# Optimization experiments

Measured on AMD Instinct MI355X. Metric: run time of the kernel, lower is better.

Reference implementation:

```python
import jax, jax.numpy as jnp
import numpy as np

# Module config (mirrors SWTLayer(__init__) with dimensions=[64,64,16], kmax=[3,3], wavelet='db1')
DIMS = (64, 64)      # spatial sizes along axes 1,2
LEVELS = (6, 6)      # pywt.dwt_max_level(64, dec_len=2) == 6 (Haar)
KMAX = (3, 3)
NLIFT = 16
BATCH = 32


def swt_haar(x, level, axis):
    """pywt.swt(x, 'db1', level, trim_approx=True, norm=True) along `axis` (periodic).
    norm=True Haar level-j step s=2^(j-1): cA[i]=(a[i]+a[i+s])/2, cD[i]=(a[i]-a[i+s])/2.
    Returns concat([cA_n, cD_n, ..., cD_1]) along axis (length (level+1)*M)."""
    a = x
    details = []
    for j in range(level):
        s = 2 ** j
        sh = jnp.roll(a, -s, axis)   # a[i + s] (periodic)
        details.append((a - sh) * 0.5)
        a = (a + sh) * 0.5
    return jnp.concatenate([a] + details[::-1], axis=axis)


def iswt_haar(xt, level, axis):
    """pywt.iswt inverse of swt_haar: averages the two phase reconstructions per level."""
    bands = jnp.split(xt, level + 1, axis=axis)  # [cA_n, cD_n, ..., cD_1]
    a = bands[0]
    for j in range(level, 0, -1):
        cD = bands[level - j + 1]
        s = 2 ** (j - 1)
        a = 0.5 * ((a + cD) + jnp.roll(a - cD, s, axis))
    return a


def setup_inputs() -> dict:
    key = jax.random.key(0)
    k1, k2, k3 = jax.random.split(key, 3)
    x = jax.random.normal(k1, (BATCH, DIMS[0], DIMS[1], NLIFT), dtype=jnp.float32)
    W = jax.random.uniform(
        k2,
        (NLIFT, NLIFT, DIMS[0] * (LEVELS[0] + 1), DIMS[1] * (LEVELS[1] + 1)),
        dtype=jnp.float32,
    )
    b = jax.random.normal(k3, (NLIFT, NLIFT), dtype=jnp.float32)
    return {"x": x, "weights": W, "bias": b}


def reference(x, weights, bias):
    # forward SWT along each spatial axis -> (B, 448, 448, C)
    xt = x
    for i, L in enumerate(LEVELS):
        xt = swt_haar(xt, L, axis=i + 1)
    # truncate: zero wavenumber bands [kmax*M, level*M) along each spatial axis
    for i, (M, L, K) in enumerate(zip(DIMS, LEVELS, KMAX)):
        idx = (slice(None),) * (i + 1) + (slice(K * M, L * M),)
        xt = xt.at[idx].set(0.0)
    # per-location channel mixing: 'abcd,debc->abce'
    xt = jnp.einsum('abcd,debc->abce', xt, weights)
    # inverse SWT back to (B, 64, 64, C)
    out = xt
    for i, L in enumerate(LEVELS):
        out = iswt_haar(out, L, axis=i + 1)
    # skip path: F.linear(x, bias) == x @ bias.T
    return out + x @ bias.T
```

## Files before the change

### kernel.cpp

```cpp
#include <hip/hip_runtime.h>
#include <cstddef>
#include <cstdint>


#define X1_IDX(a,u,j,d) ((((size_t)(a)*256 + (u))*64 + (j))*16 + (d))

__global__ __launch_bounds__(64) void k_swt1(const float* __restrict__ x,
                                             float* __restrict__ X1) {
  const int tid = threadIdx.x;
  const int d = tid & 15, jl = tid >> 4;
  const int a = blockIdx.x;
  const int j = blockIdx.y * 4 + jl;
  __shared__ float col[64 * 64];
  const float* xp = x + ((size_t)a * 4096 + j) * 16 + d;
  float S = 0.f;
  for (int i = 0; i < 64; ++i) {
    float v = xp[(size_t)i * 1024];
    col[i * 64 + tid] = v;
    S += v;
  }
  const float cA = S * 0.015625f;
  float w4 = 0.f, w4b = 0.f;
  for (int t = 0; t < 16; ++t)  w4  += col[t * 64 + tid];
  for (int t = 16; t < 32; ++t) w4b += col[t * 64 + tid];
  float w5 = w4 + w4b;
  float* X1p = X1 + X1_IDX(a, 0, j, d);
  for (int u = 0; u < 64; ++u) {
    const float c0 = col[u * 64 + tid];
    const float c16 = col[((u + 16) & 63) * 64 + tid];
    const float c32 = col[((u + 32) & 63) * 64 + tid];
    const float c1 = col[((u + 1) & 63) * 64 + tid];
    X1p[(size_t)(u) * 1024]        = cA;
    X1p[(size_t)(64 + u) * 1024]   = w5 * 0.03125f - cA;
    X1p[(size_t)(128 + u) * 1024]  = (w4 - w4b) * 0.03125f;
    X1p[(size_t)(192 + u) * 1024]  = (c0 - c1) * 0.5f;
    w4 += c16 - c0;
    w4b += c32 - c16;
    w5 += c32 - c0;
  }
}

#define APB 8
#define TS_STRIDE 4104
#define TS(a,v,d) ((a) * TS_STRIDE + (v) * 16 + (d))
#define WL_STRIDE 264

__global__ __launch_bounds__(256, 1) void k_fused(float* __restrict__ X1,
                                                  const float* __restrict__ W) {
  const int t = threadIdx.x;
  const int a0 = blockIdx.x * APB;
  const int u = blockIdx.y;
  const int ub = u >> 6;
  const int Brow = (ub == 3 ? 6 : ub) * 64 + (u & 63);
  __shared__ float Ts[APB * TS_STRIDE];
  __shared__ float Wl[16 * WL_STRIDE];

  if (t < 128) {
    const int a = t >> 4, d = t & 15;
    const float* xp = X1 + X1_IDX(a0 + a, u, 0, d);
    float raw[64];
    float S = 0.f, w4 = 0.f, w4b = 0.f;
#pragma unroll
    for (int j = 0; j < 64; ++j) {
      raw[j] = xp[j * 16];
      S += raw[j];
    }
#pragma unroll
    for (int j = 0; j < 16; ++j) w4 += raw[j];
#pragma unroll
    for (int j = 16; j < 32; ++j) w4b += raw[j];
    const float cA = S * 0.015625f;
    float w5 = w4 + w4b;
#pragma unroll
    for (int v = 0; v < 64; ++v) {
      Ts[TS(a, v, d)]       = cA;
      Ts[TS(a, 64 + v, d)]  = w5 * 0.03125f - cA;
      Ts[TS(a, 128 + v, d)] = (w4 - w4b) * 0.03125f;
      Ts[TS(a, 192 + v, d)] = (raw[v] - raw[(v + 1) & 63]) * 0.5f;
      const float c0 = raw[v], c16 = raw[(v + 16) & 63], c32 = raw[(v + 32) & 63];
      w4 += c16 - c0;
      w4b += c32 - c16;
      w5 += c32 - c0;
    }
  }
  __syncthreads();

  const int vl = t >> 4, e = t & 15;
  const float* wbase = W + (size_t)t * 200704 + (size_t)Brow * 448;
  for (int vg = 0; vg < 16; ++vg) {
    const int kb = vg >> 2;
    const int Ccol = (kb == 3 ? 6 : kb) * 64 + (vg & 3) * 16;
    __syncthreads();
    {
      const float* wp = wbase + Ccol;
#pragma unroll
      for (int i = 0; i < 16; i += 4) {
        float4 wv = *(const float4*)(wp + i);
        Wl[(i + 0) * WL_STRIDE + t] = wv.x;
        Wl[(i + 1) * WL_STRIDE + t] = wv.y;
        Wl[(i + 2) * WL_STRIDE + t] = wv.z;
        Wl[(i + 3) * WL_STRIDE + t] = wv.w;
      }
    }
    __syncthreads();
    const int v = vg * 16 + vl;
    float wreg[16];
#pragma unroll
    for (int d = 0; d < 16; ++d) wreg[d] = Wl[vl * WL_STRIDE + d * 16 + e];
#pragma unroll
    for (int a = 0; a < APB; ++a) {
      const float4 t0 = *(const float4*)&Ts[TS(a, v, 0)];
      const float4 t1 = *(const float4*)&Ts[TS(a, v, 4)];
      const float4 t2 = *(const float4*)&Ts[TS(a, v, 8)];
      const float4 t3 = *(const float4*)&Ts[TS(a, v, 12)];
      float acc = t0.x * wreg[0] + t0.y * wreg[1] + t0.z * wreg[2] + t0.w * wreg[3]
                + t1.x * wreg[4] + t1.y * wreg[5] + t1.z * wreg[6] + t1.w * wreg[7]
                + t2.x * wreg[8] + t2.y * wreg[9] + t2.z * wreg[10] + t2.w * wreg[11]
                + t3.x * wreg[12] + t3.y * wreg[13] + t3.z * wreg[14] + t3.w * wreg[15];
      Ts[TS(a, v, e)] = acc;
    }
  }
  __syncthreads();

  if (t < 128) {
    const int a = t >> 4, ee = t & 15;
    const float cA = Ts[TS(a, 0, ee)];
    float d6[64];
#pragma unroll
    for (int i = 0; i < 64; ++i) d6[i] = Ts[TS(a, 64 + i, ee)];
    float b6[64];
#pragma unroll
    for (int i = 0; i < 64; ++i) b6[i] = cA + 0.5f * (d6[i] - d6[(i - 32) & 63]);
    float d5[64];
#pragma unroll
    for (int i = 0; i < 64; ++i) d5[i] = Ts[TS(a, 128 + i, ee)];
    float a5[64];
#pragma unroll
    for (int i = 0; i < 64; ++i)
      a5[i] = 0.5f * (b6[i] + d5[i] + b6[(i - 16) & 63] - d5[(i - 16) & 63]);
    float b4[64];
#pragma unroll
    for (int i = 0; i < 64; ++i) b4[i] = 0.5f * (a5[i] + a5[(i - 8) & 63]);
    float a3[64];
#pragma unroll
    for (int i = 0; i < 64; ++i) a3[i] = 0.5f * (b4[i] + b4[(i - 4) & 63]);
    float b2[64];
#pragma unroll
    for (int i = 0; i < 64; ++i) b2[i] = 0.5f * (a3[i] + a3[(i - 2) & 63]);
    float d1[64];
#pragma unroll
    for (int i = 0; i < 64; ++i) d1[i] = Ts[TS(a, 192 + i, ee)];
    float* zp = X1 + X1_IDX(a0 + a, u, 0, ee);
#pragma unroll
    for (int j = 0; j < 64; ++j)
      zp[j * 16] = 0.5f * (b2[j] + d1[j] + b2[(j - 1) & 63] - d1[(j - 1) & 63]);
  }
}

__global__ __launch_bounds__(64) void k_iswt1(const float* __restrict__ Z1,
                                              const float* __restrict__ x,
                                              const float* __restrict__ bias,
                                              float* __restrict__ out) {
  const int tid = threadIdx.x, e = tid & 15, jl = tid >> 4;
  const int a = blockIdx.x, j = blockIdx.y * 4 + jl;
  __shared__ float A[64 * 64], Bv[64 * 64];
  __shared__ float bs[256];
  for (int i = tid; i < 256; i += 64) bs[i] = bias[i];
  __syncthreads();
  const float* Zp = Z1 + (size_t)a * 262144 + (size_t)j * 16 + e;
  for (int i = 0; i < 64; ++i) A[i * 64 + tid] = Zp[(size_t)i * 1024];
  for (int i = 0; i < 64; ++i) {
    float D = Zp[(size_t)(64 + i) * 1024];
    float D2 = Zp[(size_t)(64 + ((i - 32) & 63)) * 1024];
    Bv[i * 64 + tid] = 0.5f * (A[i * 64 + tid] + D + A[((i - 32) & 63) * 64 + tid] - D2);
  }
  for (int i = 0; i < 64; ++i) {
    float D = Zp[(size_t)(128 + i) * 1024];
    float D2 = Zp[(size_t)(128 + ((i - 16) & 63)) * 1024];
    A[i * 64 + tid] = 0.5f * (Bv[i * 64 + tid] + D + Bv[((i - 16) & 63) * 64 + tid] - D2);
  }
  for (int i = 0; i < 64; ++i)
    Bv[i * 64 + tid] = 0.5f * (A[i * 64 + tid] + A[((i - 8) & 63) * 64 + tid]);
  for (int i = 0; i < 64; ++i)
    A[i * 64 + tid] = 0.5f * (Bv[i * 64 + tid] + Bv[((i - 4) & 63) * 64 + tid]);
  for (int i = 0; i < 64; ++i)
    Bv[i * 64 + tid] = 0.5f * (A[i * 64 + tid] + A[((i - 2) & 63) * 64 + tid]);
  const float* xp = x + ((size_t)a * 4096 + j) * 16;
  float* op = out + ((size_t)a * 4096 + j) * 16 + e;
  for (int i = 0; i < 64; ++i) {
    float D = Zp[(size_t)(192 + i) * 1024];
    float D2 = Zp[(size_t)(192 + ((i - 1) & 63)) * 1024];
    float r = 0.5f * (Bv[i * 64 + tid] + D + Bv[((i - 1) & 63) * 64 + tid] - D2);
    float s = 0.f;
#pragma unroll
    for (int dd = 0; dd < 16; ++dd) s += xp[(size_t)i * 1024 + dd] * bs[e * 16 + dd];
    op[(size_t)i * 1024] = r + s;
  }
}

extern "C" void kernel_launch(void* const* d_in, const int* in_sizes, int n_in,
                              void* d_out, int out_size, void* d_ws, size_t ws_size,
                              hipStream_t stream) {
  const float* x = (const float*)d_in[0];
  const float* W = (const float*)d_in[1];
  const float* bias = (const float*)d_in[2];
  float* out = (float*)d_out;
  float* X1 = (float*)d_ws;

  k_swt1<<<dim3(32, 16), 64, 0, stream>>>(x, X1);
  k_fused<<<dim3(4, 256), 256, 0, stream>>>(X1, W);
  k_iswt1<<<dim3(32, 16), 64, 0, stream>>>(X1, x, bias, out);
}
```

Baseline: 401.7 us.

## Parallelize all three kernels across 256 threads and double-buffer weight loads

All three kernels are restructured. The SWT and ISWT kernels now split the 64-row transform across four thread groups of 256 threads, with partial sums shared through LDS. The fused kernel drops from 8 to 2 batch elements per block, uses a 4096-block grid with a remapped block index so blocks reuse W rows, and prefetches the next weight tile into registers while double-buffering it in LDS. The per-thread 64-register inverse transform is replaced by cooperative LDS passes, and the level 4-2 averaging collapses into an 8-tap sum. This targets low occupancy and idle threads, at the cost of more barriers and more redundant W loads per batch element.

```diff
diff --git a/kernel.cpp b/kernel.cpp
--- a/kernel.cpp
+++ b/kernel.cpp
@@ -5,196 +5,279 @@
 
 #define X1_IDX(a,u,j,d) ((((size_t)(a)*256 + (u))*64 + (j))*16 + (d))
 
-__global__ __launch_bounds__(64) void k_swt1(const float* __restrict__ x,
-                                             float* __restrict__ X1) {
-  const int tid = threadIdx.x;
-  const int d = tid & 15, jl = tid >> 4;
-  const int a = blockIdx.x;
-  const int j = blockIdx.y * 4 + jl;
+__global__ __launch_bounds__(256, 2) void k_swt1(const float* __restrict__ x,
+                                                 float* __restrict__ X1) {
   __shared__ float col[64 * 64];
-  const float* xp = x + ((size_t)a * 4096 + j) * 16 + d;
-  float S = 0.f;
-  for (int i = 0; i < 64; ++i) {
-    float v = xp[(size_t)i * 1024];
-    col[i * 64 + tid] = v;
-    S += v;
-  }
-  const float cA = S * 0.015625f;
-  float w4 = 0.f, w4b = 0.f;
-  for (int t = 0; t < 16; ++t)  w4  += col[t * 64 + tid];
-  for (int t = 16; t < 32; ++t) w4b += col[t * 64 + tid];
+  __shared__ float Ps[4][64];
+  const int t = threadIdx.x;
+  const int q = t >> 6, c = t & 63, jl = c >> 4, d = c & 15;
+  const int a = blockIdx.x, j = blockIdx.y * 4 + jl;
+  const float* xp = x + ((size_t)a * 4096 + j) * 16 + d + (size_t)(q * 16) * 1024;
+  float P = 0.f;
+#pragma unroll
+  for (int r = 0; r < 16; ++r) {
+    float v = xp[(size_t)r * 1024];
+    col[(q * 16 + r) * 64 + c] = v;
+    P += v;
+  }
+  Ps[q][c] = P;
+  __syncthreads();
+  const float cA = (Ps[0][c] + Ps[1][c] + Ps[2][c] + Ps[3][c]) * 0.015625f;
+  float w4 = Ps[q][c], w4b = Ps[(q + 1) & 3][c];
   float w5 = w4 + w4b;
   float* X1p = X1 + X1_IDX(a, 0, j, d);
-  for (int u = 0; u < 64; ++u) {
-    const float c0 = col[u * 64 + tid];
-    const float c16 = col[((u + 16) & 63) * 64 + tid];
-    const float c32 = col[((u + 32) & 63) * 64 + tid];
-    const float c1 = col[((u + 1) & 63) * 64 + tid];
-    X1p[(size_t)(u) * 1024]        = cA;
-    X1p[(size_t)(64 + u) * 1024]   = w5 * 0.03125f - cA;
-    X1p[(size_t)(128 + u) * 1024]  = (w4 - w4b) * 0.03125f;
-    X1p[(size_t)(192 + u) * 1024]  = (c0 - c1) * 0.5f;
+#pragma unroll
+  for (int r = 0; r < 16; ++r) {
+    const int u = q * 16 + r;
+    const float c0 = col[u * 64 + c];
+    const float c1 = col[((u + 1) & 63) * 64 + c];
+    const float c16 = col[((u + 16) & 63) * 64 + c];
+    const float c32 = col[((u + 32) & 63) * 64 + c];
+    X1p[(size_t)(u) * 1024]       = cA;
+    X1p[(size_t)(64 + u) * 1024]  = w5 * 0.03125f - cA;
+    X1p[(size_t)(128 + u) * 1024] = (w4 - w4b) * 0.03125f;
+    X1p[(size_t)(192 + u) * 1024] = (c0 - c1) * 0.5f;
     w4 += c16 - c0;
     w4b += c32 - c16;
     w5 += c32 - c0;
   }
 }
 
-#define APB 8
-#define TS_STRIDE 4104
-#define TS(a,v,d) ((a) * TS_STRIDE + (v) * 16 + (d))
-#define WL_STRIDE 264
-
-__global__ __launch_bounds__(256, 1) void k_fused(float* __restrict__ X1,
+#define TSS 20
+#define TSA (256 * TSS)
+#define TS2(a,v,d) ((a) * TSA + (v) * TSS + (d))
+#define WLS 18
+
+__global__ __launch_bounds__(256, 2) void k_fused(float* __restrict__ X1,
                                                   const float* __restrict__ W) {
+  __shared__ float Ts[2 * TSA];
+  __shared__ float Wl[2 * 256 * WLS];
+  __shared__ float Ps[2 * 8 * 16];
   const int t = threadIdx.x;
-  const int a0 = blockIdx.x * APB;
-  const int u = blockIdx.y;
+  const int bid = blockIdx.x;
+  const int u = (bid & 7) + 8 * (bid >> 7);
+  const int ac = (bid >> 3) & 15;
+  const int a0 = ac * 2;
   const int ub = u >> 6;
   const int Brow = (ub == 3 ? 6 : ub) * 64 + (u & 63);
-  __shared__ float Ts[APB * TS_STRIDE];
-  __shared__ float Wl[16 * WL_STRIDE];
-
-  if (t < 128) {
-    const int a = t >> 4, d = t & 15;
-    const float* xp = X1 + X1_IDX(a0 + a, u, 0, d);
-    float raw[64];
-    float S = 0.f, w4 = 0.f, w4b = 0.f;
-#pragma unroll
-    for (int j = 0; j < 64; ++j) {
-      raw[j] = xp[j * 16];
-      S += raw[j];
-    }
-#pragma unroll
-    for (int j = 0; j < 16; ++j) w4 += raw[j];
-#pragma unroll
-    for (int j = 16; j < 32; ++j) w4b += raw[j];
-    const float cA = S * 0.015625f;
+
+  const int aA = t >> 7, qA = (t >> 4) & 7, dA = t & 15;
+
+  {
+    const float* xp = X1 + X1_IDX(a0 + aA, u, qA * 8, dA);
+    float P = 0.f;
+#pragma unroll
+    for (int r = 0; r < 8; ++r) {
+      float v = xp[r * 16];
+      Ts[TS2(aA, 192 + qA * 8 + r, dA)] = v;
+      P += v;
+    }
+    Ps[aA * 128 + qA * 16 + dA] = P;
+  }
+  __syncthreads();
+  {
+    float cA = 0.f;
+#pragma unroll
+    for (int k = 0; k < 8; ++k) cA += Ps[aA * 128 + k * 16 + dA];
+    cA *= 0.015625f;
+    float w4 = Ps[aA * 128 + qA * 16 + dA] + Ps[aA * 128 + (((qA + 1) & 7) * 16) + dA];
+    float w4b = Ps[aA * 128 + (((qA + 2) & 7) * 16) + dA] + Ps[aA * 128 + (((qA + 3) & 7) * 16) + dA];
     float w5 = w4 + w4b;
-#pragma unroll
-    for (int v = 0; v < 64; ++v) {
-      Ts[TS(a, v, d)]       = cA;
-      Ts[TS(a, 64 + v, d)]  = w5 * 0.03125f - cA;
-      Ts[TS(a, 128 + v, d)] = (w4 - w4b) * 0.03125f;
-      Ts[TS(a, 192 + v, d)] = (raw[v] - raw[(v + 1) & 63]) * 0.5f;
-      const float c0 = raw[v], c16 = raw[(v + 16) & 63], c32 = raw[(v + 32) & 63];
+    float cd1[8];
+#pragma unroll
+    for (int r = 0; r < 8; ++r) {
+      const int v = qA * 8 + r;
+      const float c0 = Ts[TS2(aA, 192 + v, dA)];
+      const float c1 = Ts[TS2(aA, 192 + ((v + 1) & 63), dA)];
+      const float c16 = Ts[TS2(aA, 192 + ((v + 16) & 63), dA)];
+      const float c32 = Ts[TS2(aA, 192 + ((v + 32) & 63), dA)];
+      Ts[TS2(aA, v, dA)]       = cA;
+      Ts[TS2(aA, 64 + v, dA)]  = w5 * 0.03125f - cA;
+      Ts[TS2(aA, 128 + v, dA)] = (w4 - w4b) * 0.03125f;
+      cd1[r] = (c0 - c1) * 0.5f;
       w4 += c16 - c0;
       w4b += c32 - c16;
       w5 += c32 - c0;
     }
+    __syncthreads();
+#pragma unroll
+    for (int r = 0; r < 8; ++r) Ts[TS2(aA, 192 + qA * 8 + r, dA)] = cd1[r];
   }
   __syncthreads();
 
   const int vl = t >> 4, e = t & 15;
   const float* wbase = W + (size_t)t * 200704 + (size_t)Brow * 448;
+  float4 pw0, pw1, pw2, pw3;
+  {
+    const float* wp = wbase;
+    pw0 = *(const float4*)(wp + 0);
+    pw1 = *(const float4*)(wp + 4);
+    pw2 = *(const float4*)(wp + 8);
+    pw3 = *(const float4*)(wp + 12);
+  }
   for (int vg = 0; vg < 16; ++vg) {
-    const int kb = vg >> 2;
-    const int Ccol = (kb == 3 ? 6 : kb) * 64 + (vg & 3) * 16;
-    __syncthreads();
+    const int buf = vg & 1;
     {
-      const float* wp = wbase + Ccol;
-#pragma unroll
-      for (int i = 0; i < 16; i += 4) {
-        float4 wv = *(const float4*)(wp + i);
-        Wl[(i + 0) * WL_STRIDE + t] = wv.x;
-        Wl[(i + 1) * WL_STRIDE + t] = wv.y;
-        Wl[(i + 2) * WL_STRIDE + t] = wv.z;
-        Wl[(i + 3) * WL_STRIDE + t] = wv.w;
-      }
-    }
-    __syncthreads();
+      float* wrow = &Wl[(buf * 256 + t) * WLS];
+      *(float2*)&wrow[0]  = make_float2(pw0.x, pw0.y);
+      *(float2*)&wrow[2]  = make_float2(pw0.z, pw0.w);
+      *(float2*)&wrow[4]  = make_float2(pw1.x, pw1.y);
+      *(float2*)&wrow[6]  = make_float2(pw1.z, pw1.w);
+      *(float2*)&wrow[8]  = make_float2(pw2.x, pw2.y);
+      *(float2*)&wrow[10] = make_float2(pw2.z, pw2.w);
+      *(float2*)&wrow[12] = make_float2(pw3.x, pw3.y);
+      *(float2*)&wrow[14] = make_float2(pw3.z, pw3.w);
+    }
+    __syncthreads();
+    if (vg < 15) {
+      const int v2 = vg + 1;
+      const int kb2 = v2 >> 2;
+      const float* wp = wbase + (kb2 == 3 ? 384 : kb2 * 64) + (v2 & 3) * 16;
+      pw0 = *(const float4*)(wp + 0);
+      pw1 = *(const float4*)(wp + 4);
+      pw2 = *(const float4*)(wp + 8);
+      pw3 = *(const float4*)(wp + 12);
+    }
+    float wreg[16];
+#pragma unroll
+    for (int d = 0; d < 16; ++d)
+      wreg[d] = Wl[(buf * 256 + d * 16 + e) * WLS + vl];
     const int v = vg * 16 + vl;
-    float wreg[16];
-#pragma unroll
-    for (int d = 0; d < 16; ++d) wreg[d] = Wl[vl * WL_STRIDE + d * 16 + e];
-#pragma unroll
-    for (int a = 0; a < APB; ++a) {
-      const float4 t0 = *(const float4*)&Ts[TS(a, v, 0)];
-      const float4 t1 = *(const float4*)&Ts[TS(a, v, 4)];
-      const float4 t2 = *(const float4*)&Ts[TS(a, v, 8)];
-      const float4 t3 = *(const float4*)&Ts[TS(a, v, 12)];
+#pragma unroll
+    for (int a = 0; a < 2; ++a) {
+      const float4 t0 = *(const float4*)&Ts[TS2(a, v, 0)];
+      const float4 t1 = *(const float4*)&Ts[TS2(a, v, 4)];
+      const float4 t2 = *(const float4*)&Ts[TS2(a, v, 8)];
+      const float4 t3 = *(const float4*)&Ts[TS2(a, v, 12)];
       float acc = t0.x * wreg[0] + t0.y * wreg[1] + t0.z * wreg[2] + t0.w * wreg[3]
                 + t1.x * wreg[4] + t1.y * wreg[5] + t1.z * wreg[6] + t1.w * wreg[7]
                 + t2.x * wreg[8] + t2.y * wreg[9] + t2.z * wreg[10] + t2.w * wreg[11]
                 + t3.x * wreg[12] + t3.y * wreg[13] + t3.z * wreg[14] + t3.w * wreg[15];
-      Ts[TS(a, v, e)] = acc;
-    }
-  }
-  __syncthreads();
-
-  if (t < 128) {
-    const int a = t >> 4, ee = t & 15;
-    const float cA = Ts[TS(a, 0, ee)];
-    float d6[64];
-#pragma unroll
-    for (int i = 0; i < 64; ++i) d6[i] = Ts[TS(a, 64 + i, ee)];
-    float b6[64];
-#pragma unroll
-    for (int i = 0; i < 64; ++i) b6[i] = cA + 0.5f * (d6[i] - d6[(i - 32) & 63]);
-    float d5[64];
-#pragma unroll
-    for (int i = 0; i < 64; ++i) d5[i] = Ts[TS(a, 128 + i, ee)];
-    float a5[64];
-#pragma unroll
-    for (int i = 0; i < 64; ++i)
-      a5[i] = 0.5f * (b6[i] + d5[i] + b6[(i - 16) & 63] - d5[(i - 16) & 63]);
-    float b4[64];
-#pragma unroll
-    for (int i = 0; i < 64; ++i) b4[i] = 0.5f * (a5[i] + a5[(i - 8) & 63]);
-    float a3[64];
-#pragma unroll
-    for (int i = 0; i < 64; ++i) a3[i] = 0.5f * (b4[i] + b4[(i - 4) & 63]);
-    float b2[64];
-#pragma unroll
-    for (int i = 0; i < 64; ++i) b2[i] = 0.5f * (a3[i] + a3[(i - 2) & 63]);
-    float d1[64];
-#pragma unroll
-    for (int i = 0; i < 64; ++i) d1[i] = Ts[TS(a, 192 + i, ee)];
-    float* zp = X1 + X1_IDX(a0 + a, u, 0, ee);
-#pragma unroll
-    for (int j = 0; j < 64; ++j)
-      zp[j * 16] = 0.5f * (b2[j] + d1[j] + b2[(j - 1) & 63] - d1[(j - 1) & 63]);
-  }
-}
-
-__global__ __launch_bounds__(64) void k_iswt1(const float* __restrict__ Z1,
-                                              const float* __restrict__ x,
-                                              const float* __restrict__ bias,
-                                              float* __restrict__ out) {
-  const int tid = threadIdx.x, e = tid & 15, jl = tid >> 4;
+      Ts[TS2(a, v, e)] = acc;
+    }
+  }
+  __syncthreads();
+
+  {
+    const int aC = t >> 7, qC = (t >> 4) & 7, eC = t & 15;
+    float rg[8];
+#pragma unroll
+    for (int r = 0; r < 8; ++r) {
+      const int i = qC * 8 + r, i2 = (i - 32) & 63;
+      rg[r] = 0.5f * (Ts[TS2(aC, i, eC)] + Ts[TS2(aC, 64 + i, eC)]
+                    + Ts[TS2(aC, i2, eC)] - Ts[TS2(aC, 64 + i2, eC)]);
+    }
+    __syncthreads();
+#pragma unroll
+    for (int r = 0; r < 8; ++r) Ts[TS2(aC, qC * 8 + r, eC)] = rg[r];
+    __syncthreads();
+#pragma unroll
+    for (int r = 0; r < 8; ++r) {
+      const int i = qC * 8 + r, i2 = (i - 16) & 63;
+      rg[r] = 0.5f * (Ts[TS2(aC, i, eC)] + Ts[TS2(aC, 128 + i, eC)]
+                    + Ts[TS2(aC, i2, eC)] - Ts[TS2(aC, 128 + i2, eC)]);
+    }
+    __syncthreads();
+#pragma unroll
+    for (int r = 0; r < 8; ++r) Ts[TS2(aC, 64 + qC * 8 + r, eC)] = rg[r];
+    __syncthreads();
+#pragma unroll
+    for (int r = 0; r < 8; ++r) {
+      const int i = qC * 8 + r;
+      float s = 0.f;
+#pragma unroll
+      for (int k = 0; k < 8; ++k) s += Ts[TS2(aC, 64 + ((i - 2 * k) & 63), eC)];
+      rg[r] = s * 0.125f;
+    }
+    __syncthreads();
+#pragma unroll
+    for (int r = 0; r < 8; ++r) Ts[TS2(aC, qC * 8 + r, eC)] = rg[r];
+    __syncthreads();
+    float* zp = X1 + X1_IDX(a0 + aC, u, 0, eC);
+#pragma unroll
+    for (int r = 0; r < 8; ++r) {
+      const int i = qC * 8 + r, i2 = (i - 1) & 63;
+      zp[i * 16] = 0.5f * (Ts[TS2(aC, i, eC)] + Ts[TS2(aC, 192 + i, eC)]
+                         + Ts[TS2(aC, i2, eC)] - Ts[TS2(aC, 192 + i2, eC)]);
+    }
+  }
+}
+
+__global__ __launch_bounds__(256, 2) void k_iswt1(const float* __restrict__ Z1,
+                                                  const float* __restrict__ x,
+                                                  const float* __restrict__ bias,
+                                                  float* __restrict__ out) {
+  __shared__ float A[64 * 64], Bb[64 * 64], D[64 * 64], xs[64 * 64];
+  const int t = threadIdx.x;
+  const int q = t >> 6, c = t & 63, jl = c >> 4, e = c & 15;
   const int a = blockIdx.x, j = blockIdx.y * 4 + jl;
-  __shared__ float A[64 * 64], Bv[64 * 64];
-  __shared__ float bs[256];
-  for (int i = tid; i < 256; i += 64) bs[i] = bias[i];
-  __syncthreads();
+  float breg[16];
+  {
+    const float4 b0 = *(const float4*)&bias[e * 16 + 0];
+    const float4 b1 = *(const float4*)&bias[e * 16 + 4];
+    const float4 b2 = *(const float4*)&bias[e * 16 + 8];
+    const float4 b3 = *(const float4*)&bias[e * 16 + 12];
+    breg[0]=b0.x; breg[1]=b0.y; breg[2]=b0.z; breg[3]=b0.w;
+    breg[4]=b1.x; breg[5]=b1.y; breg[6]=b1.z; breg[7]=b1.w;
+    breg[8]=b2.x; breg[9]=b2.y; breg[10]=b2.z; breg[11]=b2.w;
+    breg[12]=b3.x; breg[13]=b3.y; breg[14]=b3.z; breg[15]=b3.w;
+  }
   const float* Zp = Z1 + (size_t)a * 262144 + (size_t)j * 16 + e;
-  for (int i = 0; i < 64; ++i) A[i * 64 + tid] = Zp[(size_t)i * 1024];
-  for (int i = 0; i < 64; ++i) {
-    float D = Zp[(size_t)(64 + i) * 1024];
-    float D2 = Zp[(size_t)(64 + ((i - 32) & 63)) * 1024];
-    Bv[i * 64 + tid] = 0.5f * (A[i * 64 + tid] + D + A[((i - 32) & 63) * 64 + tid] - D2);
-  }
-  for (int i = 0; i < 64; ++i) {
-    float D = Zp[(size_t)(128 + i) * 1024];
-    float D2 = Zp[(size_t)(128 + ((i - 16) & 63)) * 1024];
-    A[i * 64 + tid] = 0.5f * (Bv[i * 64 + tid] + D + Bv[((i - 16) & 63) * 64 + tid] - D2);
-  }
-  for (int i = 0; i < 64; ++i)
-    Bv[i * 64 + tid] = 0.5f * (A[i * 64 + tid] + A[((i - 8) & 63) * 64 + tid]);
-  for (int i = 0; i < 64; ++i)
-    A[i * 64 + tid] = 0.5f * (Bv[i * 64 + tid] + Bv[((i - 4) & 63) * 64 + tid]);
-  for (int i = 0; i < 64; ++i)
-    Bv[i * 64 + tid] = 0.5f * (A[i * 64 + tid] + A[((i - 2) & 63) * 64 + tid]);
-  const float* xp = x + ((size_t)a * 4096 + j) * 16;
-  float* op = out + ((size_t)a * 4096 + j) * 16 + e;
-  for (int i = 0; i < 64; ++i) {
-    float D = Zp[(size_t)(192 + i) * 1024];
-    float D2 = Zp[(size_t)(192 + ((i - 1) & 63)) * 1024];
-    float r = 0.5f * (Bv[i * 64 + tid] + D + Bv[((i - 1) & 63) * 64 + tid] - D2);
+#pragma unroll
+  for (int r = 0; r < 16; ++r) {
+    const int i = q * 16 + r;
+    A[i * 64 + c] = Zp[(size_t)i * 1024];
+    D[i * 64 + c] = Zp[(size_t)(64 + i) * 1024];
+    xs[i * 64 + c] = x[((size_t)a * 4096 + (size_t)i * 64 + j) * 16 + e];
+  }
+  __syncthreads();
+  float rg[16];
+#pragma unroll
+  for (int r = 0; r < 16; ++r) {
+    const int i = q * 16 + r, i2 = (i - 32) & 63;
+    rg[r] = 0.5f * (A[i * 64 + c] + D[i * 64 + c] + A[i2 * 64 + c] - D[i2 * 64 + c]);
+  }
+  __syncthreads();
+#pragma unroll
+  for (int r = 0; r < 16; ++r) {
+    const int i = q * 16 + r;
+    Bb[i * 64 + c] = rg[r];
+    D[i * 64 + c] = Zp[(size_t)(128 + i) * 1024];
+  }
+  __syncthreads();
+#pragma unroll
+  for (int r = 0; r < 16; ++r) {
+    const int i = q * 16 + r, i2 = (i - 16) & 63;
+    rg[r] = 0.5f * (Bb[i * 64 + c] + D[i * 64 + c] + Bb[i2 * 64 + c] - D[i2 * 64 + c]);
+  }
+  __syncthreads();
+#pragma unroll
+  for (int r = 0; r < 16; ++r) {
+    const int i = q * 16 + r;
+    A[i * 64 + c] = rg[r];
+    D[i * 64 + c] = Zp[(size_t)(192 + i) * 1024];
+  }
+  __syncthreads();
+#pragma unroll
+  for (int r = 0; r < 16; ++r) {
+    const int i = q * 16 + r;
     float s = 0.f;
 #pragma unroll
-    for (int dd = 0; dd < 16; ++dd) s += xp[(size_t)i * 1024 + dd] * bs[e * 16 + dd];
-    op[(size_t)i * 1024] = r + s;
+    for (int k = 0; k < 8; ++k) s += A[((i - 2 * k) & 63) * 64 + c];
+    rg[r] = s * 0.125f;
+  }
+  __syncthreads();
+#pragma unroll
+  for (int r = 0; r < 16; ++r) Bb[(q * 16 + r) * 64 + c] = rg[r];
+  __syncthreads();
+#pragma unroll
+  for (int r = 0; r < 16; ++r) {
+    const int i = q * 16 + r, i2 = (i - 1) & 63;
+    float v = 0.5f * (Bb[i * 64 + c] + D[i * 64 + c] + Bb[i2 * 64 + c] - D[i2 * 64 + c]);
+    float s = 0.f;
+#pragma unroll
+    for (int dd = 0; dd < 16; ++dd) s += xs[i * 64 + jl * 16 + dd] * breg[dd];
+    out[((size_t)a * 4096 + (size_t)i * 64 + j) * 16 + e] = v + s;
   }
 }
 
@@ -207,7 +290,7 @@
   float* out = (float*)d_out;
   float* X1 = (float*)d_ws;
 
-  k_swt1<<<dim3(32, 16), 64, 0, stream>>>(x, X1);
-  k_fused<<<dim3(4, 256), 256, 0, stream>>>(X1, W);
-  k_iswt1<<<dim3(32, 16), 64, 0, stream>>>(X1, x, bias, out);
-}
+  k_swt1<<<dim3(32, 16), 256, 0, stream>>>(x, X1);
+  k_fused<<<dim3(4096), 256, 0, stream>>>(X1, W);
+  k_iswt1<<<dim3(32, 16), 256, 0, stream>>>(X1, x, bias, out);
+}
```

Result: slower. 421.0 us (+4.8%).
